# Performance work log

Hardware: AMD Instinct MI355X
Metric: run time of the kernel (lower is better)

The kernel has to match this reference:

```python
import jax, jax.numpy as jnp
import numpy as np

EMB = 2048
NH = 16
HD = EMB // NH
EPS = 1e-5


def setup_inputs() -> dict:
    key = jax.random.key(0)
    ks = jax.random.split(key, 16)
    s = 1.0 / np.sqrt(EMB)
    def lin(k, din, dout):
        return jax.random.normal(k, (din, dout), jnp.float32) * (1.0 / np.sqrt(din))
    return {
        "embeddings": jax.random.normal(ks[0], (2, 2048, EMB), jnp.float32),
        "Wq": lin(ks[1], EMB, EMB), "bq": jnp.zeros((EMB,), jnp.float32),
        "Wk": lin(ks[2], EMB, EMB), "bk": jnp.zeros((EMB,), jnp.float32),
        "Wv": lin(ks[3], EMB, EMB), "bv": jnp.zeros((EMB,), jnp.float32),
        "Wfc": lin(ks[4], EMB, EMB), "bfc": jnp.zeros((EMB,), jnp.float32),
        "g1": jnp.ones((EMB,), jnp.float32), "be1": jnp.zeros((EMB,), jnp.float32),
        "W1": lin(ks[5], EMB, 4 * EMB), "b1": jnp.zeros((4 * EMB,), jnp.float32),
        "W2": lin(ks[6], 4 * EMB, EMB), "b2": jnp.zeros((EMB,), jnp.float32),
        "g2": jnp.ones((EMB,), jnp.float32), "be2": jnp.zeros((EMB,), jnp.float32),
    }


def _layernorm(x, g, b):
    mu = jnp.mean(x, axis=-1, keepdims=True)
    var = jnp.mean(jnp.square(x - mu), axis=-1, keepdims=True)
    return (x - mu) * jax.lax.rsqrt(var + EPS) * g + b


def reference(embeddings, Wq, bq, Wk, bk, Wv, bv, Wfc, bfc, g1, be1, W1, b1, W2, b2, g2, be2):
    B, S, E = embeddings.shape
    old = embeddings
    # QKV projections, split heads: [B, H, S, D]
    def heads(x):
        return x.reshape(B, S, NH, HD).transpose(0, 2, 1, 3)
    q = heads(embeddings @ Wq + bq)
    k = heads(embeddings @ Wk + bk)
    v = heads(embeddings @ Wv + bv)
    # naive causal attention: full [B,H,S,S] scores (faithful to source)
    scores = jnp.einsum("bhsd,bhtd->bhst", q, k) / np.sqrt(HD)
    causal = jnp.triu(jnp.full((S, S), -jnp.inf, jnp.float32), k=1)
    scores = scores + causal[None, None]
    attn = jax.nn.softmax(scores, axis=-1)
    ctx = jnp.einsum("bhst,bhtd->bhsd", attn, v)
    ctx = ctx.transpose(0, 2, 1, 3).reshape(B, S, E)
    # dropout is identity in eval mode
    x = ctx @ Wfc + bfc + old
    old = _layernorm(x, g1, be1)
    h = jax.nn.gelu(old @ W1 + b1, approximate=False)
    x = h @ W2 + b2 + old
    return _layernorm(x, g2, be2)
```

## Files before the change

kernel.cpp:

```cpp
#include <hip/hip_runtime.h>
#include <hip/hip_bf16.h>
#include <math.h>

#define EMB  2048
#define NH   16
#define HD   128
#define SEQ  2048
#define BATCH 2
#define MTOK (BATCH*SEQ)

using bf16x8 = __attribute__((ext_vector_type(8))) __bf16;
using f32x4  = __attribute__((ext_vector_type(4))) float;

__device__ __forceinline__ unsigned short f2bf(float x) {
    unsigned int u = __float_as_uint(x);
    u += 0x7fffu + ((u >> 16) & 1u);
    return (unsigned short)(u >> 16);
}

__device__ __forceinline__ float gelu_exact(float x) {
    return 0.5f * x * (1.0f + erff(x * 0.70710678118654752f));
}

__global__ __launch_bounds__(256) void k_conv(const float* __restrict__ in,
                                              unsigned short* __restrict__ out, int n4) {
    int i = blockIdx.x * 256 + threadIdx.x;
    if (i >= n4) return;
    float4 v = ((const float4*)in)[i];
    ushort4 o;
    o.x = f2bf(v.x); o.y = f2bf(v.y); o.z = f2bf(v.z); o.w = f2bf(v.w);
    ((ushort4*)out)[i] = o;
}

__global__ __launch_bounds__(256) void k_transconv(const float* __restrict__ W,
                                                   unsigned short* __restrict__ Wt,
                                                   int K, int N) {
    __shared__ float t[32][33];
    int tx = threadIdx.x & 31, ty = threadIdx.x >> 5;
    int c0 = blockIdx.x * 32, r0 = blockIdx.y * 32;
    #pragma unroll
    for (int i = 0; i < 4; ++i)
        t[ty + i*8][tx] = W[(size_t)(r0 + ty + i*8) * N + c0 + tx];
    __syncthreads();
    #pragma unroll
    for (int i = 0; i < 4; ++i)
        Wt[(size_t)(c0 + ty + i*8) * K + r0 + tx] = f2bf(t[tx][ty + i*8]);
}

template<int EPI, int NSPLIT>
__global__ __launch_bounds__(512, 1) void k_gemm3(const unsigned short* __restrict__ A,
                                                  const unsigned short* __restrict__ Bt,
                                                  const float* __restrict__ bias,
                                                  void* __restrict__ C0,
                                                  void* __restrict__ C1,
                                                  void* __restrict__ C2,
                                                  int M, int N, int Kred, int ldk) {
    __shared__ unsigned short As[2][256 * 64];
    __shared__ unsigned short Bs[2][256 * 64];
    const int tid = threadIdx.x, lane = tid & 63, wid = tid >> 6;
    const int wm = wid >> 2, wn = wid & 3;
    const int nmt = M >> 8, nnt = N >> 8;
    const int nblk = nmt * nnt * NSPLIT, cpx = nblk >> 3;
    const int swz = (blockIdx.x & 7) * cpx + (blockIdx.x >> 3);
    const int bm = swz % nmt;
    const int t2 = swz / nmt;
    const int bn = t2 % nnt, kk = t2 / nnt;
    const unsigned short* Ab = A  + (size_t)bm * 256 * ldk + (size_t)kk * Kred;
    const unsigned short* Bb = Bt + (size_t)bn * 256 * ldk + (size_t)kk * Kred;

    auto STAGE = [&](int ti, int bbuf) {
        const int kt = ti * 64;
        #pragma unroll
        for (int it = 0; it < 4; ++it) {
            const int slot = it * 512 + tid;
            const int r = slot >> 3, cs = slot & 7;
            const unsigned short* ga = Ab + (size_t)r * ldk + kt + ((cs ^ (r & 7)) * 8);
            __builtin_amdgcn_global_load_lds(
                (const __attribute__((address_space(1))) void*)ga,
                (__attribute__((address_space(3))) void*)&As[bbuf][(it*512 + wid*64) * 8], 16, 0, 0);
            const unsigned short* gb = Bb + (size_t)r * ldk + kt + ((cs ^ (r & 7)) * 8);
            __builtin_amdgcn_global_load_lds(
                (const __attribute__((address_space(1))) void*)gb,
                (__attribute__((address_space(3))) void*)&Bs[bbuf][(it*512 + wid*64) * 8], 16, 0, 0);
        }
    };

    f32x4 acc[8][4] = {};
    const int NT = Kred >> 6;
    STAGE(0, 0);
    STAGE(1, 1);

    for (int t = 0; t < NT; ++t) {
        const int bb = t & 1;
        if (t == NT - 1) asm volatile("s_waitcnt vmcnt(0)" ::: "memory");
        else             asm volatile("s_waitcnt vmcnt(8)" ::: "memory");
        __builtin_amdgcn_s_barrier();
        __builtin_amdgcn_sched_barrier(0);

        #pragma unroll
        for (int kh = 0; kh < 2; ++kh) {
            bf16x8 af[8], bfr[4];
            #pragma unroll
            for (int mi = 0; mi < 8; ++mi)
                af[mi] = *(const bf16x8*)&As[bb][(wm*128 + mi*16 + (lane & 15))*64
                                                + (((kh*4 + (lane >> 4)) ^ (lane & 7)) * 8)];
            #pragma unroll
            for (int ni = 0; ni < 4; ++ni)
                bfr[ni] = *(const bf16x8*)&Bs[bb][(wn*64 + ni*16 + (lane & 15))*64
                                                 + (((kh*4 + (lane >> 4)) ^ (lane & 7)) * 8)];
            __builtin_amdgcn_s_setprio(1);
            #pragma unroll
            for (int mi = 0; mi < 8; ++mi)
                #pragma unroll
                for (int ni = 0; ni < 4; ++ni)
                    acc[mi][ni] = __builtin_amdgcn_mfma_f32_16x16x32_bf16(af[mi], bfr[ni], acc[mi][ni], 0, 0, 0);
            __builtin_amdgcn_s_setprio(0);
            __builtin_amdgcn_sched_barrier(0);
        }

        __builtin_amdgcn_s_barrier();
        __builtin_amdgcn_sched_barrier(0);
        if (t + 2 < NT) STAGE(t + 2, bb);
    }

    const int row0b = bm*256 + wm*128, col0 = bn*256 + wn*64;
    #pragma unroll
    for (int mi = 0; mi < 8; ++mi) {
        #pragma unroll
        for (int ni = 0; ni < 4; ++ni) {
            const int c = col0 + ni*16 + (lane & 15);
            const int r0 = row0b + mi*16 + (lane >> 4) * 4;
            if (EPI == 5) {
                float* out = (float*)C0 + (size_t)kk * M * N;
                #pragma unroll
                for (int j = 0; j < 4; ++j)
                    out[(size_t)(r0+j) * N + c] = acc[mi][ni][j];
            } else if (EPI == 2) {
                const float bv = bias[c];
                #pragma unroll
                for (int j = 0; j < 4; ++j)
                    ((unsigned short*)C0)[(size_t)(r0+j) * N + c] = f2bf(gelu_exact(acc[mi][ni][j] + bv));
            } else {
                const float bv = bias[c];
                const int seg = c >> 11;
                if (seg == 0) {
                    #pragma unroll
                    for (int j = 0; j < 4; ++j)
                        ((unsigned short*)C0)[(size_t)(r0+j) * EMB + c] = f2bf(acc[mi][ni][j] + bv);
                } else if (seg == 1) {
                    #pragma unroll
                    for (int j = 0; j < 4; ++j)
                        ((unsigned short*)C1)[(size_t)(r0+j) * EMB + (c - 2048)] = f2bf(acc[mi][ni][j] + bv);
                } else {
                    const int cc = c - 4096;
                    const int hh = cc >> 7, dd = cc & 127;
                    const int bb2 = r0 >> 11, s0 = r0 & 2047;
                    ushort4 u;
                    u.x = f2bf(acc[mi][ni][0] + bv); u.y = f2bf(acc[mi][ni][1] + bv);
                    u.z = f2bf(acc[mi][ni][2] + bv); u.w = f2bf(acc[mi][ni][3] + bv);
                    *(ushort4*)((unsigned short*)C2 +
                                ((size_t)((bb2*NH + hh)*HD + dd) * SEQ + s0)) = u;
                }
            }
        }
    }
}

__global__ __launch_bounds__(256, 4) void k_attn_part(const unsigned short* __restrict__ Qb,
                                                      const unsigned short* __restrict__ Kb,
                                                      const unsigned short* __restrict__ VTb,
                                                      float* __restrict__ Opart,
                                                      float* __restrict__ Ml) {
    const int tid = threadIdx.x;
    const int lane = tid & 63, w = tid >> 6;
    const int g = lane >> 4, c = lane & 15;
    const int bid = blockIdx.x;
    const int swz = (bid & 7) * 512 + (bid >> 3);
    const int bh = swz >> 7;
    const int b = bh >> 4, h = bh & 15;
    const int rr = swz & 127;
    const int qt = rr >> 2, ks = rr & 3;
    const int nt = qt + 1;
    const int t0 = (nt * ks) >> 2, t1 = (nt * (ks + 1)) >> 2;
    const int qb = qt * 64 + w * 16;

    __shared__ unsigned short Ks[64 * 128];
    __shared__ unsigned short Vs[128 * 64];
    __shared__ unsigned short p_lds[4][16 * 64];

    bf16x8 qf[4];
    {
        const unsigned short* qrow = Qb + (size_t)(b*SEQ + qb + c) * EMB + h*HD;
        #pragma unroll
        for (int dch = 0; dch < 4; ++dch)
            qf[dch] = *(const bf16x8*)(qrow + dch*32 + g*8);
    }

    f32x4 o[8];
    #pragma unroll
    for (int ni = 0; ni < 8; ++ni) o[ni] = (f32x4){0.f, 0.f, 0.f, 0.f};
    float m_c = -1e30f, l_c = 0.f;

    const int q = qb + c;
    const int qmaxw = qb + 15;
    const unsigned short* Kbase = Kb  + (size_t)(b*SEQ) * EMB + h*HD;
    const unsigned short* Vbase = VTb + (size_t)((b*NH + h) * HD) * SEQ;
    const float scale = 0.08838834764831845f;
    char* pw = (char*)&p_lds[w][0];

    for (int ti = t0; ti < t1; ++ti) {
        const int tc = ti * 64;
        #pragma unroll
        for (int it = 0; it < 4; ++it) {
            const int cl = it * 256 + tid;
            const unsigned short* gk = Kbase + (size_t)(tc + (cl >> 4)) * EMB
                                     + (((cl & 15) ^ ((cl >> 4) & 7)) * 8);
            __builtin_amdgcn_global_load_lds(
                (const __attribute__((address_space(1))) void*)gk,
                (__attribute__((address_space(3))) void*)&Ks[(it*256 + w*64) * 8], 16, 0, 0);
            const unsigned short* gv = Vbase + (size_t)(cl >> 3) * SEQ + tc
                                     + (((cl & 7) ^ ((cl >> 3) & 7)) * 8);
            __builtin_amdgcn_global_load_lds(
                (const __attribute__((address_space(1))) void*)gv,
                (__attribute__((address_space(3))) void*)&Vs[(it*256 + w*64) * 8], 16, 0, 0);
        }
        __syncthreads();

        f32x4 sc[4];
        #pragma unroll
        for (int kt = 0; kt < 4; ++kt) {
            sc[kt] = (f32x4){0.f, 0.f, 0.f, 0.f};
            if (tc + kt*16 <= qmaxw) {
                #pragma unroll
                for (int dch = 0; dch < 4; ++dch) {
                    bf16x8 kf = *(const bf16x8*)&Ks[(kt*16 + c)*128 + (((dch*4 + g) ^ (c & 7)) * 8)];
                    sc[kt] = __builtin_amdgcn_mfma_f32_16x16x32_bf16(kf, qf[dch], sc[kt], 0, 0, 0);
                }
            }
        }
        float mx = -1e30f;
        #pragma unroll
        for (int kt = 0; kt < 4; ++kt)
            #pragma unroll
            for (int j = 0; j < 4; ++j) {
                const int key = tc + kt*16 + g*4 + j;
                const float s = (key <= q) ? sc[kt][j] * scale : -1e30f;
                mx = fmaxf(mx, s);
            }
        mx = fmaxf(mx, __shfl_xor(mx, 16));
        mx = fmaxf(mx, __shfl_xor(mx, 32));
        if (!__all(mx <= m_c + 8.f)) {
            const float mn = fmaxf(m_c, mx);
            const float corr = __expf(m_c - mn);
            l_c *= corr;
            m_c = mn;
            #pragma unroll
            for (int j = 0; j < 4; ++j) {
                const float cj = __shfl(corr, g*4 + j);
                #pragma unroll
                for (int ni = 0; ni < 8; ++ni) o[ni][j] *= cj;
            }
        }
        float ps = 0.f;
        #pragma unroll
        for (int kt = 0; kt < 4; ++kt) {
            float p[4];
            #pragma unroll
            for (int j = 0; j < 4; ++j) {
                const int key = tc + kt*16 + g*4 + j;
                const float s = (key <= q) ? sc[kt][j] * scale : -1e30f;
                p[j] = __expf(s - m_c);
                ps += p[j];
            }
            uint2 pk;
            pk.x = (unsigned int)f2bf(p[0]) | ((unsigned int)f2bf(p[1]) << 16);
            pk.y = (unsigned int)f2bf(p[2]) | ((unsigned int)f2bf(p[3]) << 16);
            const int byte = (c*128 + kt*32 + g*8) ^ ((c & 7) << 4);
            *(uint2*)(pw + byte) = pk;
        }
        ps += __shfl_xor(ps, 16);
        ps += __shfl_xor(ps, 32);
        l_c += ps;
        asm volatile("s_waitcnt lgkmcnt(0)" ::: "memory");
        __builtin_amdgcn_sched_barrier(0);
        #pragma unroll
        for (int kc = 0; kc < 2; ++kc) {
            if (tc + kc*32 <= qmaxw) {
                const int byte = (c*128 + kc*64 + g*16) ^ ((c & 7) << 4);
                bf16x8 pa = *(const bf16x8*)(pw + byte);
                #pragma unroll
                for (int ni = 0; ni < 8; ++ni) {
                    bf16x8 vf = *(const bf16x8*)&Vs[(ni*16 + c)*64 + (((kc*4 + g) ^ (c & 7)) * 8)];
                    o[ni] = __builtin_amdgcn_mfma_f32_16x16x32_bf16(pa, vf, o[ni], 0, 0, 0);
                }
            }
        }
        __syncthreads();
    }

    const int slot = ((b*NH + h) * 32 + qt) * 4 + ks;
    float* op = Opart + (size_t)slot * (64 * 128);
    #pragma unroll
    for (int ni = 0; ni < 8; ++ni)
        #pragma unroll
        for (int j = 0; j < 4; ++j)
            op[(size_t)(w*16 + g*4 + j) * 128 + ni*16 + c] = o[ni][j];
    if (lane < 16) {
        Ml[(size_t)slot * 128 +      w*16 + lane] = m_c;
        Ml[(size_t)slot * 128 + 64 + w*16 + lane] = l_c;
    }
}

__global__ __launch_bounds__(256) void k_attn_reduce(const float* __restrict__ Opart,
                                                     const float* __restrict__ Ml,
                                                     unsigned short* __restrict__ Ob) {
    const int qt = blockIdx.x, h = blockIdx.y, b = blockIdx.z;
    const int slot0 = ((b*NH + h) * 32 + qt) * 4;
    const int row = threadIdx.x >> 2;
    const int c0 = (threadIdx.x & 3) * 32;
    float M = -1e30f;
    #pragma unroll
    for (int s = 0; s < 4; ++s)
        M = fmaxf(M, Ml[(size_t)(slot0 + s) * 128 + row]);
    float L = 0.f;
    float wgt[4];
    #pragma unroll
    for (int s = 0; s < 4; ++s) {
        wgt[s] = __expf(Ml[(size_t)(slot0 + s) * 128 + row] - M);
        L += Ml[(size_t)(slot0 + s) * 128 + 64 + row] * wgt[s];
    }
    float acc[32];
    #pragma unroll
    for (int k = 0; k < 32; ++k) acc[k] = 0.f;
    #pragma unroll
    for (int s = 0; s < 4; ++s) {
        const float4* op = (const float4*)(Opart + ((size_t)(slot0 + s) * 64 + row) * 128 + c0);
        #pragma unroll
        for (int q4 = 0; q4 < 8; ++q4) {
            float4 v = op[q4];
            acc[q4*4+0] += v.x * wgt[s]; acc[q4*4+1] += v.y * wgt[s];
            acc[q4*4+2] += v.z * wgt[s]; acc[q4*4+3] += v.w * wgt[s];
        }
    }
    const float inv = 1.0f / L;
    unsigned short* orow = Ob + (size_t)(b*SEQ + qt*64 + row) * EMB + h*HD + c0;
    #pragma unroll
    for (int q4 = 0; q4 < 8; ++q4) {
        ushort4 u;
        u.x = f2bf(acc[q4*4+0] * inv); u.y = f2bf(acc[q4*4+1] * inv);
        u.z = f2bf(acc[q4*4+2] * inv); u.w = f2bf(acc[q4*4+3] * inv);
        ((ushort4*)orow)[q4] = u;
    }
}

__global__ __launch_bounds__(256) void k_ln(const float* __restrict__ X0,
                                            const float* __restrict__ X1,
                                            const float* __restrict__ bias,
                                            const float* __restrict__ res,
                                            const float* __restrict__ g,
                                            const float* __restrict__ be,
                                            float* __restrict__ Of32,
                                            unsigned short* __restrict__ Obf16) {
    const int row = blockIdx.x;
    float4 v[2];
    float s = 0.f, ss = 0.f;
    #pragma unroll
    for (int i = 0; i < 2; ++i) {
        const int c4 = threadIdx.x + i*256;
        float4 a = ((const float4*)(X0 + (size_t)row * EMB))[c4];
        if (X1) {
            float4 b1v = ((const float4*)(X1 + (size_t)row * EMB))[c4];
            a.x += b1v.x; a.y += b1v.y; a.z += b1v.z; a.w += b1v.w;
        }
        if (bias) {
            float4 bv = ((const float4*)bias)[c4];
            a.x += bv.x; a.y += bv.y; a.z += bv.z; a.w += bv.w;
        }
        if (res) {
            float4 rv = ((const float4*)(res + (size_t)row * EMB))[c4];
            a.x += rv.x; a.y += rv.y; a.z += rv.z; a.w += rv.w;
        }
        v[i] = a;
        s  += a.x + a.y + a.z + a.w;
        ss += a.x*a.x + a.y*a.y + a.z*a.z + a.w*a.w;
    }
    #pragma unroll
    for (int o = 32; o; o >>= 1) { s += __shfl_xor(s, o); ss += __shfl_xor(ss, o); }
    __shared__ float red[2][4];
    const int lane = threadIdx.x & 63, wid = threadIdx.x >> 6;
    if (lane == 0) { red[0][wid] = s; red[1][wid] = ss; }
    __syncthreads();
    s  = red[0][0] + red[0][1] + red[0][2] + red[0][3];
    ss = red[1][0] + red[1][1] + red[1][2] + red[1][3];
    const float mu = s * (1.0f / EMB);
    const float var = ss * (1.0f / EMB) - mu * mu;
    const float rs = rsqrtf(var + 1e-5f);
    #pragma unroll
    for (int i = 0; i < 2; ++i) {
        const int c4 = threadIdx.x + i*256;
        float4 gv = ((const float4*)g)[c4];
        float4 bv = ((const float4*)be)[c4];
        float4 y;
        y.x = (v[i].x - mu) * rs * gv.x + bv.x;
        y.y = (v[i].y - mu) * rs * gv.y + bv.y;
        y.z = (v[i].z - mu) * rs * gv.z + bv.z;
        y.w = (v[i].w - mu) * rs * gv.w + bv.w;
        if (Of32)  ((float4*)(Of32 + (size_t)row * EMB))[c4] = y;
        if (Obf16) {
            ushort4 u; u.x = f2bf(y.x); u.y = f2bf(y.y); u.z = f2bf(y.z); u.w = f2bf(y.w);
            ((ushort4*)(Obf16 + (size_t)row * EMB))[c4] = u;
        }
    }
}

extern "C" void kernel_launch(void* const* d_in, const int* in_sizes, int n_in,
                              void* d_out, int out_size, void* d_ws, size_t ws_size,
                              hipStream_t stream) {
    const float* emb = (const float*)d_in[0];
    const float* Wq  = (const float*)d_in[1];  const float* bq  = (const float*)d_in[2];
    const float* Wk  = (const float*)d_in[3];  const float* bk  = (const float*)d_in[4];
    const float* Wv  = (const float*)d_in[5];  const float* bv  = (const float*)d_in[6];
    const float* Wfc = (const float*)d_in[7];  const float* bfc = (const float*)d_in[8];
    const float* g1  = (const float*)d_in[9];  const float* be1 = (const float*)d_in[10];
    const float* W1  = (const float*)d_in[11]; const float* b1  = (const float*)d_in[12];
    const float* W2  = (const float*)d_in[13]; const float* b2  = (const float*)d_in[14];
    const float* g2  = (const float*)d_in[15]; const float* be2 = (const float*)d_in[16];

    char* ws = (char*)d_ws;
    unsigned short* aB   = (unsigned short*)(ws + (size_t)  0 * (1u<<20));
    unsigned short* ln1B = (unsigned short*)(ws + (size_t) 16 * (1u<<20));
    unsigned short* WtB  = (unsigned short*)(ws + (size_t) 32 * (1u<<20));
    float*          Ml   = (float*)         (ws + (size_t) 32 * (1u<<20));
    unsigned short* hB   = (unsigned short*)(ws + (size_t) 64 * (1u<<20));
    unsigned short* Qb   = (unsigned short*)(ws + (size_t) 64 * (1u<<20));
    unsigned short* Kb   = (unsigned short*)(ws + (size_t) 80 * (1u<<20));
    unsigned short* VTb  = (unsigned short*)(ws + (size_t) 96 * (1u<<20));
    float*          Opart= (float*)         (ws + (size_t)112 * (1u<<20));
    float*          pA   = (float*)         (ws + (size_t)128 * (1u<<20));
    float*          ln1f = (float*)         (ws + (size_t)192 * (1u<<20));
    float*          bias6= (float*)         (ws + (size_t)236 * (1u<<20));

    const dim3 blk(256);
    const dim3 blk2(512);
    const int n4 = MTOK * EMB / 4;

    k_conv<<<dim3(n4 / 256), blk, 0, stream>>>(emb, aB, n4);
    hipMemcpyAsync(bias6,        bq, EMB*sizeof(float), hipMemcpyDeviceToDevice, stream);
    hipMemcpyAsync(bias6 + EMB,  bk, EMB*sizeof(float), hipMemcpyDeviceToDevice, stream);
    hipMemcpyAsync(bias6 + 2*EMB,bv, EMB*sizeof(float), hipMemcpyDeviceToDevice, stream);

    k_transconv<<<dim3(EMB/32, EMB/32), blk, 0, stream>>>(Wq, WtB,              EMB, EMB);
    k_transconv<<<dim3(EMB/32, EMB/32), blk, 0, stream>>>(Wk, WtB + EMB*EMB,    EMB, EMB);
    k_transconv<<<dim3(EMB/32, EMB/32), blk, 0, stream>>>(Wv, WtB + 2*EMB*EMB,  EMB, EMB);
    k_gemm3<6,1><<<dim3((MTOK/256)*(3*EMB/256)), blk2, 0, stream>>>(
        aB, WtB, bias6, Qb, Kb, VTb, MTOK, 3*EMB, EMB, EMB);

    k_attn_part<<<dim3(4096), blk, 0, stream>>>(Qb, Kb, VTb, Opart, Ml);
    k_attn_reduce<<<dim3(SEQ/64, NH, BATCH), blk, 0, stream>>>(Opart, Ml, aB);

    k_transconv<<<dim3(EMB/32, EMB/32), blk, 0, stream>>>(Wfc, WtB, EMB, EMB);
    k_gemm3<5,2><<<dim3((MTOK/256)*(EMB/256)*2), blk2, 0, stream>>>(
        aB, WtB, nullptr, pA, nullptr, nullptr, MTOK, EMB, EMB/2, EMB);
    k_ln<<<dim3(MTOK), blk, 0, stream>>>(pA, pA + (size_t)MTOK*EMB, bfc, emb, g1, be1, ln1f, ln1B);

    k_transconv<<<dim3(4*EMB/32, EMB/32), blk, 0, stream>>>(W1, WtB, EMB, 4*EMB);
    k_gemm3<2,1><<<dim3((MTOK/256)*(4*EMB/256)), blk2, 0, stream>>>(
        ln1B, WtB, b1, hB, nullptr, nullptr, MTOK, 4*EMB, EMB, EMB);

    k_transconv<<<dim3(EMB/32, (4*EMB)/32), blk, 0, stream>>>(W2, WtB, 4*EMB, EMB);
    k_gemm3<5,2><<<dim3((MTOK/256)*(EMB/256)*2), blk2, 0, stream>>>(
        hB, WtB, nullptr, pA, nullptr, nullptr, MTOK, EMB, 2*EMB, 4*EMB);
    k_ln<<<dim3(MTOK), blk, 0, stream>>>(pA, pA + (size_t)MTOK*EMB, b2, ln1f, g2, be2, (float*)d_out, nullptr);
}
```

Baseline: 818.4 us.

## Split GEMM K-tile into half-stages with interleaved load/MFMA ping-pong schedule

```diff
diff --git a/kernel.cpp b/kernel.cpp
--- a/kernel.cpp
+++ b/kernel.cpp
@@ -55,8 +55,8 @@
                                                   void* __restrict__ C1,
                                                   void* __restrict__ C2,
                                                   int M, int N, int Kred, int ldk) {
-    __shared__ unsigned short As[2][256 * 64];
-    __shared__ unsigned short Bs[2][256 * 64];
+    __shared__ unsigned short As[2][2][256 * 32];
+    __shared__ unsigned short Bs[2][2][256 * 32];
     const int tid = threadIdx.x, lane = tid & 63, wid = tid >> 6;
     const int wm = wid >> 2, wn = wid & 3;
     const int nmt = M >> 8, nnt = N >> 8;
@@ -64,63 +64,117 @@
     const int swz = (blockIdx.x & 7) * cpx + (blockIdx.x >> 3);
     const int bm = swz % nmt;
     const int t2 = swz / nmt;
-    const int bn = t2 % nnt, kk = t2 / nnt;
-    const unsigned short* Ab = A  + (size_t)bm * 256 * ldk + (size_t)kk * Kred;
-    const unsigned short* Bb = Bt + (size_t)bn * 256 * ldk + (size_t)kk * Kred;
-
-    auto STAGE = [&](int ti, int bbuf) {
-        const int kt = ti * 64;
-        #pragma unroll
-        for (int it = 0; it < 4; ++it) {
-            const int slot = it * 512 + tid;
-            const int r = slot >> 3, cs = slot & 7;
-            const unsigned short* ga = Ab + (size_t)r * ldk + kt + ((cs ^ (r & 7)) * 8);
-            __builtin_amdgcn_global_load_lds(
-                (const __attribute__((address_space(1))) void*)ga,
-                (__attribute__((address_space(3))) void*)&As[bbuf][(it*512 + wid*64) * 8], 16, 0, 0);
-            const unsigned short* gb = Bb + (size_t)r * ldk + kt + ((cs ^ (r & 7)) * 8);
-            __builtin_amdgcn_global_load_lds(
-                (const __attribute__((address_space(1))) void*)gb,
-                (__attribute__((address_space(3))) void*)&Bs[bbuf][(it*512 + wid*64) * 8], 16, 0, 0);
-        }
+    const int bn = t2 % nnt, kk2 = t2 / nnt;
+    const unsigned short* Ab = A  + (size_t)bm * 256 * ldk + (size_t)kk2 * Kred;
+    const unsigned short* Bb = Bt + (size_t)bn * 256 * ldk + (size_t)kk2 * Kred;
+
+    const int sr0 = tid >> 2,        sc0 = (tid & 3) ^ ((sr0 >> 1) & 3);
+    const int sr1 = (512 + tid) >> 2, sc1 = ((512 + tid) & 3) ^ ((sr1 >> 1) & 3);
+
+    auto STAGE = [&](const unsigned short* gb, int u, int kh, unsigned short* lds) {
+        const int kb = u * 64 + kh * 32;
+        __builtin_amdgcn_global_load_lds(
+            (const __attribute__((address_space(1))) void*)(gb + (size_t)sr0 * ldk + kb + sc0 * 8),
+            (__attribute__((address_space(3))) void*)&lds[(size_t)wid * 64 * 8], 16, 0, 0);
+        __builtin_amdgcn_global_load_lds(
+            (const __attribute__((address_space(1))) void*)(gb + (size_t)sr1 * ldk + kb + sc1 * 8),
+            (__attribute__((address_space(3))) void*)&lds[(size_t)(512 + wid * 64) * 8], 16, 0, 0);
     };
+
+    const int ck   = (((lane >> 4) ^ ((lane >> 1) & 3)) * 8);
+    const int la15 = lane & 15;
 
     f32x4 acc[8][4] = {};
     const int NT = Kred >> 6;
-    STAGE(0, 0);
-    STAGE(1, 1);
-
-    for (int t = 0; t < NT; ++t) {
-        const int bb = t & 1;
-        if (t == NT - 1) asm volatile("s_waitcnt vmcnt(0)" ::: "memory");
-        else             asm volatile("s_waitcnt vmcnt(8)" ::: "memory");
-        __builtin_amdgcn_s_barrier();
-        __builtin_amdgcn_sched_barrier(0);
-
-        #pragma unroll
-        for (int kh = 0; kh < 2; ++kh) {
-            bf16x8 af[8], bfr[4];
-            #pragma unroll
-            for (int mi = 0; mi < 8; ++mi)
-                af[mi] = *(const bf16x8*)&As[bb][(wm*128 + mi*16 + (lane & 15))*64
-                                                + (((kh*4 + (lane >> 4)) ^ (lane & 7)) * 8)];
-            #pragma unroll
-            for (int ni = 0; ni < 4; ++ni)
-                bfr[ni] = *(const bf16x8*)&Bs[bb][(wn*64 + ni*16 + (lane & 15))*64
-                                                 + (((kh*4 + (lane >> 4)) ^ (lane & 7)) * 8)];
-            __builtin_amdgcn_s_setprio(1);
-            #pragma unroll
-            for (int mi = 0; mi < 8; ++mi)
-                #pragma unroll
-                for (int ni = 0; ni < 4; ++ni)
-                    acc[mi][ni] = __builtin_amdgcn_mfma_f32_16x16x32_bf16(af[mi], bfr[ni], acc[mi][ni], 0, 0, 0);
-            __builtin_amdgcn_s_setprio(0);
-            __builtin_amdgcn_sched_barrier(0);
-        }
-
-        __builtin_amdgcn_s_barrier();
-        __builtin_amdgcn_sched_barrier(0);
-        if (t + 2 < NT) STAGE(t + 2, bb);
+
+    STAGE(Ab, 0, 0, &As[0][0][0]);
+    STAGE(Bb, 0, 0, &Bs[0][0][0]);
+    STAGE(Ab, 0, 1, &As[0][1][0]);
+    STAGE(Bb, 0, 1, &Bs[0][1][0]);
+    asm volatile("s_waitcnt vmcnt(4)" ::: "memory");
+    __builtin_amdgcn_s_barrier();
+
+    for (int u = 0; u < NT; ++u) {
+        const int cur = u & 1, nb = cur ^ 1;
+        const bool more = (u + 1 < NT);
+        bf16x8 af[8], bfr[4];
+
+        #pragma unroll
+        for (int mi = 0; mi < 8; ++mi)
+            af[mi] = *(const bf16x8*)&As[cur][0][(wm*128 + mi*16 + la15)*32 + ck];
+        bfr[0] = *(const bf16x8*)&Bs[cur][0][(wn*64 +  0 + la15)*32 + ck];
+        bfr[1] = *(const bf16x8*)&Bs[cur][0][(wn*64 + 16 + la15)*32 + ck];
+        if (more) STAGE(Ab, u + 1, 0, &As[nb][0][0]);
+        __builtin_amdgcn_sched_barrier(0);
+        __builtin_amdgcn_s_barrier();
+        asm volatile("s_waitcnt lgkmcnt(0)" ::: "memory");
+        __builtin_amdgcn_sched_barrier(0);
+        __builtin_amdgcn_s_setprio(1);
+        #pragma unroll
+        for (int mi = 0; mi < 8; ++mi) {
+            acc[mi][0] = __builtin_amdgcn_mfma_f32_16x16x32_bf16(af[mi], bfr[0], acc[mi][0], 0, 0, 0);
+            acc[mi][1] = __builtin_amdgcn_mfma_f32_16x16x32_bf16(af[mi], bfr[1], acc[mi][1], 0, 0, 0);
+        }
+        __builtin_amdgcn_s_setprio(0);
+        __builtin_amdgcn_sched_barrier(0);
+        __builtin_amdgcn_s_barrier();
+
+        bfr[2] = *(const bf16x8*)&Bs[cur][0][(wn*64 + 32 + la15)*32 + ck];
+        bfr[3] = *(const bf16x8*)&Bs[cur][0][(wn*64 + 48 + la15)*32 + ck];
+        if (more) STAGE(Bb, u + 1, 0, &Bs[nb][0][0]);
+        __builtin_amdgcn_sched_barrier(0);
+        __builtin_amdgcn_s_barrier();
+        asm volatile("s_waitcnt lgkmcnt(0)" ::: "memory");
+        __builtin_amdgcn_sched_barrier(0);
+        __builtin_amdgcn_s_setprio(1);
+        #pragma unroll
+        for (int mi = 0; mi < 8; ++mi) {
+            acc[mi][2] = __builtin_amdgcn_mfma_f32_16x16x32_bf16(af[mi], bfr[2], acc[mi][2], 0, 0, 0);
+            acc[mi][3] = __builtin_amdgcn_mfma_f32_16x16x32_bf16(af[mi], bfr[3], acc[mi][3], 0, 0, 0);
+        }
+        __builtin_amdgcn_s_setprio(0);
+        __builtin_amdgcn_sched_barrier(0);
+        if (more) asm volatile("s_waitcnt vmcnt(4)" ::: "memory");
+        else      asm volatile("s_waitcnt vmcnt(0)" ::: "memory");
+        __builtin_amdgcn_s_barrier();
+
+        #pragma unroll
+        for (int mi = 0; mi < 8; ++mi)
+            af[mi] = *(const bf16x8*)&As[cur][1][(wm*128 + mi*16 + la15)*32 + ck];
+        bfr[0] = *(const bf16x8*)&Bs[cur][1][(wn*64 +  0 + la15)*32 + ck];
+        bfr[1] = *(const bf16x8*)&Bs[cur][1][(wn*64 + 16 + la15)*32 + ck];
+        if (more) STAGE(Ab, u + 1, 1, &As[nb][1][0]);
+        __builtin_amdgcn_sched_barrier(0);
+        __builtin_amdgcn_s_barrier();
+        asm volatile("s_waitcnt lgkmcnt(0)" ::: "memory");
+        __builtin_amdgcn_sched_barrier(0);
+        __builtin_amdgcn_s_setprio(1);
+        #pragma unroll
+        for (int mi = 0; mi < 8; ++mi) {
+            acc[mi][0] = __builtin_amdgcn_mfma_f32_16x16x32_bf16(af[mi], bfr[0], acc[mi][0], 0, 0, 0);
+            acc[mi][1] = __builtin_amdgcn_mfma_f32_16x16x32_bf16(af[mi], bfr[1], acc[mi][1], 0, 0, 0);
+        }
+        __builtin_amdgcn_s_setprio(0);
+        __builtin_amdgcn_sched_barrier(0);
+        __builtin_amdgcn_s_barrier();
+
+        bfr[2] = *(const bf16x8*)&Bs[cur][1][(wn*64 + 32 + la15)*32 + ck];
+        bfr[3] = *(const bf16x8*)&Bs[cur][1][(wn*64 + 48 + la15)*32 + ck];
+        if (more) STAGE(Bb, u + 1, 1, &Bs[nb][1][0]);
+        __builtin_amdgcn_sched_barrier(0);
+        __builtin_amdgcn_s_barrier();
+        asm volatile("s_waitcnt lgkmcnt(0)" ::: "memory");
+        __builtin_amdgcn_sched_barrier(0);
+        __builtin_amdgcn_s_setprio(1);
+        #pragma unroll
+        for (int mi = 0; mi < 8; ++mi) {
+            acc[mi][2] = __builtin_amdgcn_mfma_f32_16x16x32_bf16(af[mi], bfr[2], acc[mi][2], 0, 0, 0);
+            acc[mi][3] = __builtin_amdgcn_mfma_f32_16x16x32_bf16(af[mi], bfr[3], acc[mi][3], 0, 0, 0);
+        }
+        __builtin_amdgcn_s_setprio(0);
+        __builtin_amdgcn_sched_barrier(0);
+        asm volatile("s_waitcnt vmcnt(4)" ::: "memory");
+        __builtin_amdgcn_s_barrier();
     }
 
     const int row0b = bm*256 + wm*128, col0 = bn*256 + wn*64;
@@ -128,10 +182,10 @@
     for (int mi = 0; mi < 8; ++mi) {
         #pragma unroll
         for (int ni = 0; ni < 4; ++ni) {
-            const int c = col0 + ni*16 + (lane & 15);
+            const int c = col0 + ni*16 + la15;
             const int r0 = row0b + mi*16 + (lane >> 4) * 4;
             if (EPI == 5) {
-                float* out = (float*)C0 + (size_t)kk * M * N;
+                float* out = (float*)C0 + (size_t)kk2 * M * N;
                 #pragma unroll
                 for (int j = 0; j < 4; ++j)
                     out[(size_t)(r0+j) * N + c] = acc[mi][ni][j];
@@ -155,11 +209,11 @@
                     const int cc = c - 4096;
                     const int hh = cc >> 7, dd = cc & 127;
                     const int bb2 = r0 >> 11, s0 = r0 & 2047;
-                    ushort4 u;
-                    u.x = f2bf(acc[mi][ni][0] + bv); u.y = f2bf(acc[mi][ni][1] + bv);
-                    u.z = f2bf(acc[mi][ni][2] + bv); u.w = f2bf(acc[mi][ni][3] + bv);
+                    ushort4 uo;
+                    uo.x = f2bf(acc[mi][ni][0] + bv); uo.y = f2bf(acc[mi][ni][1] + bv);
+                    uo.z = f2bf(acc[mi][ni][2] + bv); uo.w = f2bf(acc[mi][ni][3] + bv);
                     *(ushort4*)((unsigned short*)C2 +
-                                ((size_t)((bb2*NH + hh)*HD + dd) * SEQ + s0)) = u;
+                                ((size_t)((bb2*NH + hh)*HD + dd) * SEQ + s0)) = uo;
                 }
             }
         }
```

Result: no change. 830.5 us (+1.5%).

## Pre-pack weights into MFMA fragment layout and load B directly to registers

Applied to the files above, without the earlier changes.

```diff
diff --git a/kernel.cpp b/kernel.cpp
--- a/kernel.cpp
+++ b/kernel.cpp
@@ -32,9 +32,9 @@
     ((ushort4*)out)[i] = o;
 }
 
-__global__ __launch_bounds__(256) void k_transconv(const float* __restrict__ W,
-                                                   unsigned short* __restrict__ Wt,
-                                                   int K, int N) {
+__global__ __launch_bounds__(256) void k_transpack(const float* __restrict__ W,
+                                                   unsigned short* __restrict__ Bp,
+                                                   int K, int N, int noff) {
     __shared__ float t[32][33];
     int tx = threadIdx.x & 31, ty = threadIdx.x >> 5;
     int c0 = blockIdx.x * 32, r0 = blockIdx.y * 32;
@@ -42,85 +42,110 @@
     for (int i = 0; i < 4; ++i)
         t[ty + i*8][tx] = W[(size_t)(r0 + ty + i*8) * N + c0 + tx];
     __syncthreads();
-    #pragma unroll
-    for (int i = 0; i < 4; ++i)
-        Wt[(size_t)(c0 + ty + i*8) * K + r0 + tx] = f2bf(t[tx][ty + i*8]);
+    const int kc = r0 >> 5;
+    #pragma unroll
+    for (int i = 0; i < 4; ++i) {
+        const int ng = noff + c0 + ty + i*8;
+        Bp[((size_t)(ng >> 4) * (K >> 5) + kc) * 512 + (ng & 15) * 32 + tx] =
+            f2bf(t[tx][ty + i*8]);
+    }
 }
 
 template<int EPI, int NSPLIT>
-__global__ __launch_bounds__(512, 1) void k_gemm3(const unsigned short* __restrict__ A,
-                                                  const unsigned short* __restrict__ Bt,
+__global__ __launch_bounds__(512, 1) void k_gemm4(const unsigned short* __restrict__ A,
+                                                  const unsigned short* __restrict__ Bp,
                                                   const float* __restrict__ bias,
                                                   void* __restrict__ C0,
                                                   void* __restrict__ C1,
                                                   void* __restrict__ C2,
                                                   int M, int N, int Kred, int ldk) {
     __shared__ unsigned short As[2][256 * 64];
-    __shared__ unsigned short Bs[2][256 * 64];
     const int tid = threadIdx.x, lane = tid & 63, wid = tid >> 6;
+    const int la15 = lane & 15, g = lane >> 4;
     const int wm = wid >> 2, wn = wid & 3;
     const int nmt = M >> 8, nnt = N >> 8;
     const int nblk = nmt * nnt * NSPLIT, cpx = nblk >> 3;
     const int swz = (blockIdx.x & 7) * cpx + (blockIdx.x >> 3);
     const int bm = swz % nmt;
     const int t2 = swz / nmt;
-    const int bn = t2 % nnt, kk = t2 / nnt;
-    const unsigned short* Ab = A  + (size_t)bm * 256 * ldk + (size_t)kk * Kred;
-    const unsigned short* Bb = Bt + (size_t)bn * 256 * ldk + (size_t)kk * Kred;
-
-    auto STAGE = [&](int ti, int bbuf) {
-        const int kt = ti * 64;
+    const int bn = t2 % nnt, kk2 = t2 / nnt;
+    const unsigned short* Ab = A + (size_t)bm * 256 * ldk + (size_t)kk2 * Kred;
+    const int nkc = ldk >> 5;
+    const unsigned short* Bptr = Bp + ((size_t)(bn*16 + wn*4) * nkc + ((kk2 * Kred) >> 5)) * 512
+                               + la15 * 32 + g * 8;
+
+    auto STAGE_A = [&](int tt, int bbuf) {
+        const int kt = tt * 64;
         #pragma unroll
         for (int it = 0; it < 4; ++it) {
-            const int slot = it * 512 + tid;
-            const int r = slot >> 3, cs = slot & 7;
-            const unsigned short* ga = Ab + (size_t)r * ldk + kt + ((cs ^ (r & 7)) * 8);
+            const int r = it * 64 + (tid >> 3);
+            const int cs = (tid & 7) ^ (r & 7);
             __builtin_amdgcn_global_load_lds(
-                (const __attribute__((address_space(1))) void*)ga,
+                (const __attribute__((address_space(1))) void*)(Ab + (size_t)r * ldk + kt + cs * 8),
                 (__attribute__((address_space(3))) void*)&As[bbuf][(it*512 + wid*64) * 8], 16, 0, 0);
-            const unsigned short* gb = Bb + (size_t)r * ldk + kt + ((cs ^ (r & 7)) * 8);
-            __builtin_amdgcn_global_load_lds(
-                (const __attribute__((address_space(1))) void*)gb,
-                (__attribute__((address_space(3))) void*)&Bs[bbuf][(it*512 + wid*64) * 8], 16, 0, 0);
-        }
+        }
+    };
+
+    bf16x8 bregA[4], bregB[4];
+    auto BLOADA = [&](int tt, int kh) {
+        #pragma unroll
+        for (int ni = 0; ni < 4; ++ni)
+            bregA[ni] = *(const bf16x8*)(Bptr + ((size_t)ni * nkc + tt*2 + kh) * 512);
+    };
+    auto BLOADB = [&](int tt, int kh) {
+        #pragma unroll
+        for (int ni = 0; ni < 4; ++ni)
+            bregB[ni] = *(const bf16x8*)(Bptr + ((size_t)ni * nkc + tt*2 + kh) * 512);
     };
 
     f32x4 acc[8][4] = {};
     const int NT = Kred >> 6;
-    STAGE(0, 0);
-    STAGE(1, 1);
+
+    STAGE_A(0, 0);
+    __builtin_amdgcn_sched_barrier(0);
+    BLOADA(0, 0);
+    __builtin_amdgcn_sched_barrier(0);
+    STAGE_A(1, 1);
+    asm volatile("s_waitcnt vmcnt(8)" ::: "memory");
+    __builtin_amdgcn_s_barrier();
 
     for (int t = 0; t < NT; ++t) {
-        const int bb = t & 1;
-        if (t == NT - 1) asm volatile("s_waitcnt vmcnt(0)" ::: "memory");
-        else             asm volatile("s_waitcnt vmcnt(8)" ::: "memory");
-        __builtin_amdgcn_s_barrier();
-        __builtin_amdgcn_sched_barrier(0);
-
-        #pragma unroll
-        for (int kh = 0; kh < 2; ++kh) {
-            bf16x8 af[8], bfr[4];
-            #pragma unroll
-            for (int mi = 0; mi < 8; ++mi)
-                af[mi] = *(const bf16x8*)&As[bb][(wm*128 + mi*16 + (lane & 15))*64
-                                                + (((kh*4 + (lane >> 4)) ^ (lane & 7)) * 8)];
+        const int cur = t & 1;
+        if (t + 1 < NT) asm volatile("s_waitcnt vmcnt(4)" ::: "memory");
+        else            asm volatile("s_waitcnt vmcnt(0)" ::: "memory");
+
+        BLOADB(t, 1);
+
+        bf16x8 af[8];
+        #pragma unroll
+        for (int mi = 0; mi < 8; ++mi)
+            af[mi] = *(const bf16x8*)&As[cur][(wm*128 + mi*16 + la15)*64 + ((g ^ (lane & 7)) * 8)];
+        __builtin_amdgcn_s_setprio(1);
+        #pragma unroll
+        for (int mi = 0; mi < 8; ++mi)
             #pragma unroll
             for (int ni = 0; ni < 4; ++ni)
-                bfr[ni] = *(const bf16x8*)&Bs[bb][(wn*64 + ni*16 + (lane & 15))*64
-                                                 + (((kh*4 + (lane >> 4)) ^ (lane & 7)) * 8)];
-            __builtin_amdgcn_s_setprio(1);
+                acc[mi][ni] = __builtin_amdgcn_mfma_f32_16x16x32_bf16(af[mi], bregA[ni], acc[mi][ni], 0, 0, 0);
+        __builtin_amdgcn_s_setprio(0);
+
+        asm volatile("s_waitcnt vmcnt(0)" ::: "memory");
+
+        #pragma unroll
+        for (int mi = 0; mi < 8; ++mi)
+            af[mi] = *(const bf16x8*)&As[cur][(wm*128 + mi*16 + la15)*64 + (((4 + g) ^ (lane & 7)) * 8)];
+        __builtin_amdgcn_s_setprio(1);
+        #pragma unroll
+        for (int mi = 0; mi < 8; ++mi)
             #pragma unroll
-            for (int mi = 0; mi < 8; ++mi)
-                #pragma unroll
-                for (int ni = 0; ni < 4; ++ni)
-                    acc[mi][ni] = __builtin_amdgcn_mfma_f32_16x16x32_bf16(af[mi], bfr[ni], acc[mi][ni], 0, 0, 0);
-            __builtin_amdgcn_s_setprio(0);
-            __builtin_amdgcn_sched_barrier(0);
-        }
-
+            for (int ni = 0; ni < 4; ++ni)
+                acc[mi][ni] = __builtin_amdgcn_mfma_f32_16x16x32_bf16(af[mi], bregB[ni], acc[mi][ni], 0, 0, 0);
+        __builtin_amdgcn_s_setprio(0);
+
+        __builtin_amdgcn_sched_barrier(0);
         __builtin_amdgcn_s_barrier();
+        if (t + 1 < NT) BLOADA(t + 1, 0);
         __builtin_amdgcn_sched_barrier(0);
-        if (t + 2 < NT) STAGE(t + 2, bb);
+        if (t + 2 < NT) STAGE_A(t + 2, cur);
     }
 
     const int row0b = bm*256 + wm*128, col0 = bn*256 + wn*64;
@@ -128,10 +153,10 @@
     for (int mi = 0; mi < 8; ++mi) {
         #pragma unroll
         for (int ni = 0; ni < 4; ++ni) {
-            const int c = col0 + ni*16 + (lane & 15);
-            const int r0 = row0b + mi*16 + (lane >> 4) * 4;
+            const int c = col0 + ni*16 + la15;
+            const int r0 = row0b + mi*16 + g * 4;
             if (EPI == 5) {
-                float* out = (float*)C0 + (size_t)kk * M * N;
+                float* out = (float*)C0 + (size_t)kk2 * M * N;
                 #pragma unroll
                 for (int j = 0; j < 4; ++j)
                     out[(size_t)(r0+j) * N + c] = acc[mi][ni][j];
@@ -155,11 +180,11 @@
                     const int cc = c - 4096;
                     const int hh = cc >> 7, dd = cc & 127;
                     const int bb2 = r0 >> 11, s0 = r0 & 2047;
-                    ushort4 u;
-                    u.x = f2bf(acc[mi][ni][0] + bv); u.y = f2bf(acc[mi][ni][1] + bv);
-                    u.z = f2bf(acc[mi][ni][2] + bv); u.w = f2bf(acc[mi][ni][3] + bv);
+                    ushort4 uo;
+                    uo.x = f2bf(acc[mi][ni][0] + bv); uo.y = f2bf(acc[mi][ni][1] + bv);
+                    uo.z = f2bf(acc[mi][ni][2] + bv); uo.w = f2bf(acc[mi][ni][3] + bv);
                     *(ushort4*)((unsigned short*)C2 +
-                                ((size_t)((bb2*NH + hh)*HD + dd) * SEQ + s0)) = u;
+                                ((size_t)((bb2*NH + hh)*HD + dd) * SEQ + s0)) = uo;
                 }
             }
         }
@@ -449,26 +474,26 @@
     hipMemcpyAsync(bias6 + EMB,  bk, EMB*sizeof(float), hipMemcpyDeviceToDevice, stream);
     hipMemcpyAsync(bias6 + 2*EMB,bv, EMB*sizeof(float), hipMemcpyDeviceToDevice, stream);
 
-    k_transconv<<<dim3(EMB/32, EMB/32), blk, 0, stream>>>(Wq, WtB,              EMB, EMB);
-    k_transconv<<<dim3(EMB/32, EMB/32), blk, 0, stream>>>(Wk, WtB + EMB*EMB,    EMB, EMB);
-    k_transconv<<<dim3(EMB/32, EMB/32), blk, 0, stream>>>(Wv, WtB + 2*EMB*EMB,  EMB, EMB);
-    k_gemm3<6,1><<<dim3((MTOK/256)*(3*EMB/256)), blk2, 0, stream>>>(
+    k_transpack<<<dim3(EMB/32, EMB/32), blk, 0, stream>>>(Wq, WtB, EMB, EMB, 0);
+    k_transpack<<<dim3(EMB/32, EMB/32), blk, 0, stream>>>(Wk, WtB, EMB, EMB, 2048);
+    k_transpack<<<dim3(EMB/32, EMB/32), blk, 0, stream>>>(Wv, WtB, EMB, EMB, 4096);
+    k_gemm4<6,1><<<dim3((MTOK/256)*(3*EMB/256)), blk2, 0, stream>>>(
         aB, WtB, bias6, Qb, Kb, VTb, MTOK, 3*EMB, EMB, EMB);
 
     k_attn_part<<<dim3(4096), blk, 0, stream>>>(Qb, Kb, VTb, Opart, Ml);
     k_attn_reduce<<<dim3(SEQ/64, NH, BATCH), blk, 0, stream>>>(Opart, Ml, aB);
 
-    k_transconv<<<dim3(EMB/32, EMB/32), blk, 0, stream>>>(Wfc, WtB, EMB, EMB);
-    k_gemm3<5,2><<<dim3((MTOK/256)*(EMB/256)*2), blk2, 0, stream>>>(
+    k_transpack<<<dim3(EMB/32, EMB/32), blk, 0, stream>>>(Wfc, WtB, EMB, EMB, 0);
+    k_gemm4<5,2><<<dim3((MTOK/256)*(EMB/256)*2), blk2, 0, stream>>>(
         aB, WtB, nullptr, pA, nullptr, nullptr, MTOK, EMB, EMB/2, EMB);
     k_ln<<<dim3(MTOK), blk, 0, stream>>>(pA, pA + (size_t)MTOK*EMB, bfc, emb, g1, be1, ln1f, ln1B);
 
-    k_transconv<<<dim3(4*EMB/32, EMB/32), blk, 0, stream>>>(W1, WtB, EMB, 4*EMB);
-    k_gemm3<2,1><<<dim3((MTOK/256)*(4*EMB/256)), blk2, 0, stream>>>(
+    k_transpack<<<dim3(4*EMB/32, EMB/32), blk, 0, stream>>>(W1, WtB, EMB, 4*EMB, 0);
+    k_gemm4<2,1><<<dim3((MTOK/256)*(4*EMB/256)), blk2, 0, stream>>>(
         ln1B, WtB, b1, hB, nullptr, nullptr, MTOK, 4*EMB, EMB, EMB);
 
-    k_transconv<<<dim3(EMB/32, (4*EMB)/32), blk, 0, stream>>>(W2, WtB, 4*EMB, EMB);
-    k_gemm3<5,2><<<dim3((MTOK/256)*(EMB/256)*2), blk2, 0, stream>>>(
+    k_transpack<<<dim3(EMB/32, (4*EMB)/32), blk, 0, stream>>>(W2, WtB, 4*EMB, EMB, 0);
+    k_gemm4<5,2><<<dim3((MTOK/256)*(EMB/256)*2), blk2, 0, stream>>>(
         hB, WtB, nullptr, pA, nullptr, nullptr, MTOK, EMB, 2*EMB, 4*EMB);
     k_ln<<<dim3(MTOK), blk, 0, stream>>>(pA, pA + (size_t)MTOK*EMB, b2, ln1f, g2, be2, (float*)d_out, nullptr);
 }
```

Result: slower. 874.0 us (+6.8%).

## Store split-K partials, attention partials and LN1 residual in bf16

Applied to the files above, without the earlier changes.

```diff
diff --git a/kernel.cpp b/kernel.cpp
--- a/kernel.cpp
+++ b/kernel.cpp
@@ -16,6 +16,9 @@
     unsigned int u = __float_as_uint(x);
     u += 0x7fffu + ((u >> 16) & 1u);
     return (unsigned short)(u >> 16);
+}
+__device__ __forceinline__ float bf2f(unsigned int u16) {
+    return __uint_as_float(u16 << 16);
 }
 
 __device__ __forceinline__ float gelu_exact(float x) {
@@ -64,9 +67,9 @@
     const int swz = (blockIdx.x & 7) * cpx + (blockIdx.x >> 3);
     const int bm = swz % nmt;
     const int t2 = swz / nmt;
-    const int bn = t2 % nnt, kk = t2 / nnt;
-    const unsigned short* Ab = A  + (size_t)bm * 256 * ldk + (size_t)kk * Kred;
-    const unsigned short* Bb = Bt + (size_t)bn * 256 * ldk + (size_t)kk * Kred;
+    const int bn = t2 % nnt, kk2 = t2 / nnt;
+    const unsigned short* Ab = A  + (size_t)bm * 256 * ldk + (size_t)kk2 * Kred;
+    const unsigned short* Bb = Bt + (size_t)bn * 256 * ldk + (size_t)kk2 * Kred;
 
     auto STAGE = [&](int ti, int bbuf) {
         const int kt = ti * 64;
@@ -131,10 +134,10 @@
             const int c = col0 + ni*16 + (lane & 15);
             const int r0 = row0b + mi*16 + (lane >> 4) * 4;
             if (EPI == 5) {
-                float* out = (float*)C0 + (size_t)kk * M * N;
+                unsigned short* out = (unsigned short*)C0 + (size_t)kk2 * M * N;
                 #pragma unroll
                 for (int j = 0; j < 4; ++j)
-                    out[(size_t)(r0+j) * N + c] = acc[mi][ni][j];
+                    out[(size_t)(r0+j) * N + c] = f2bf(acc[mi][ni][j]);
             } else if (EPI == 2) {
                 const float bv = bias[c];
                 #pragma unroll
@@ -155,11 +158,11 @@
                     const int cc = c - 4096;
                     const int hh = cc >> 7, dd = cc & 127;
                     const int bb2 = r0 >> 11, s0 = r0 & 2047;
-                    ushort4 u;
-                    u.x = f2bf(acc[mi][ni][0] + bv); u.y = f2bf(acc[mi][ni][1] + bv);
-                    u.z = f2bf(acc[mi][ni][2] + bv); u.w = f2bf(acc[mi][ni][3] + bv);
+                    ushort4 uo;
+                    uo.x = f2bf(acc[mi][ni][0] + bv); uo.y = f2bf(acc[mi][ni][1] + bv);
+                    uo.z = f2bf(acc[mi][ni][2] + bv); uo.w = f2bf(acc[mi][ni][3] + bv);
                     *(ushort4*)((unsigned short*)C2 +
-                                ((size_t)((bb2*NH + hh)*HD + dd) * SEQ + s0)) = u;
+                                ((size_t)((bb2*NH + hh)*HD + dd) * SEQ + s0)) = uo;
                 }
             }
         }
@@ -169,7 +172,7 @@
 __global__ __launch_bounds__(256, 4) void k_attn_part(const unsigned short* __restrict__ Qb,
                                                       const unsigned short* __restrict__ Kb,
                                                       const unsigned short* __restrict__ VTb,
-                                                      float* __restrict__ Opart,
+                                                      unsigned short* __restrict__ Opart,
                                                       float* __restrict__ Ml) {
     const int tid = threadIdx.x;
     const int lane = tid & 63, w = tid >> 6;
@@ -299,19 +302,19 @@
     }
 
     const int slot = ((b*NH + h) * 32 + qt) * 4 + ks;
-    float* op = Opart + (size_t)slot * (64 * 128);
+    unsigned short* op = Opart + (size_t)slot * (64 * 128);
     #pragma unroll
     for (int ni = 0; ni < 8; ++ni)
         #pragma unroll
         for (int j = 0; j < 4; ++j)
-            op[(size_t)(w*16 + g*4 + j) * 128 + ni*16 + c] = o[ni][j];
+            op[(size_t)(w*16 + g*4 + j) * 128 + ni*16 + c] = f2bf(o[ni][j]);
     if (lane < 16) {
         Ml[(size_t)slot * 128 +      w*16 + lane] = m_c;
         Ml[(size_t)slot * 128 + 64 + w*16 + lane] = l_c;
     }
 }
 
-__global__ __launch_bounds__(256) void k_attn_reduce(const float* __restrict__ Opart,
+__global__ __launch_bounds__(256) void k_attn_reduce(const unsigned short* __restrict__ Opart,
                                                      const float* __restrict__ Ml,
                                                      unsigned short* __restrict__ Ob) {
     const int qt = blockIdx.x, h = blockIdx.y, b = blockIdx.z;
@@ -334,12 +337,16 @@
     for (int k = 0; k < 32; ++k) acc[k] = 0.f;
     #pragma unroll
     for (int s = 0; s < 4; ++s) {
-        const float4* op = (const float4*)(Opart + ((size_t)(slot0 + s) * 64 + row) * 128 + c0);
-        #pragma unroll
-        for (int q4 = 0; q4 < 8; ++q4) {
-            float4 v = op[q4];
-            acc[q4*4+0] += v.x * wgt[s]; acc[q4*4+1] += v.y * wgt[s];
-            acc[q4*4+2] += v.z * wgt[s]; acc[q4*4+3] += v.w * wgt[s];
+        const unsigned short* op = Opart + ((size_t)(slot0 + s) * 64 + row) * 128 + c0;
+        #pragma unroll
+        for (int q4 = 0; q4 < 4; ++q4) {
+            uint4 u = ((const uint4*)op)[q4];
+            const unsigned int* pu = (const unsigned int*)&u;
+            #pragma unroll
+            for (int k = 0; k < 4; ++k) {
+                acc[q4*8 + 2*k]     += bf2f(pu[k] & 0xffffu) * wgt[s];
+                acc[q4*8 + 2*k + 1] += bf2f(pu[k] >> 16)     * wgt[s];
+            }
         }
     }
     const float inv = 1.0f / L;
@@ -353,41 +360,55 @@
     }
 }
 
-__global__ __launch_bounds__(256) void k_ln(const float* __restrict__ X0,
-                                            const float* __restrict__ X1,
-                                            const float* __restrict__ bias,
-                                            const float* __restrict__ res,
-                                            const float* __restrict__ g,
-                                            const float* __restrict__ be,
-                                            float* __restrict__ Of32,
-                                            unsigned short* __restrict__ Obf16) {
-    const int row = blockIdx.x;
-    float4 v[2];
+__global__ __launch_bounds__(256) void k_lnb(const unsigned short* __restrict__ X0,
+                                             const unsigned short* __restrict__ X1,
+                                             const float* __restrict__ bias,
+                                             const float* __restrict__ resF,
+                                             const unsigned short* __restrict__ resB,
+                                             const float* __restrict__ g,
+                                             const float* __restrict__ be,
+                                             float* __restrict__ Of32,
+                                             unsigned short* __restrict__ Obf16) {
+    const int row = blockIdx.x, t = threadIdx.x;
+    float v[8];
+    {
+        uint4 a = ((const uint4*)(X0 + (size_t)row * EMB))[t];
+        uint4 b = ((const uint4*)(X1 + (size_t)row * EMB))[t];
+        const unsigned int* pa = (const unsigned int*)&a;
+        const unsigned int* pb = (const unsigned int*)&b;
+        #pragma unroll
+        for (int i = 0; i < 4; ++i) {
+            v[2*i]   = bf2f(pa[i] & 0xffffu) + bf2f(pb[i] & 0xffffu);
+            v[2*i+1] = bf2f(pa[i] >> 16)     + bf2f(pb[i] >> 16);
+        }
+    }
+    {
+        float4 b0 = ((const float4*)bias)[t*2], b1 = ((const float4*)bias)[t*2+1];
+        v[0] += b0.x; v[1] += b0.y; v[2] += b0.z; v[3] += b0.w;
+        v[4] += b1.x; v[5] += b1.y; v[6] += b1.z; v[7] += b1.w;
+    }
+    if (resF) {
+        float4 r0 = ((const float4*)(resF + (size_t)row * EMB))[t*2];
+        float4 r1 = ((const float4*)(resF + (size_t)row * EMB))[t*2+1];
+        v[0] += r0.x; v[1] += r0.y; v[2] += r0.z; v[3] += r0.w;
+        v[4] += r1.x; v[5] += r1.y; v[6] += r1.z; v[7] += r1.w;
+    }
+    if (resB) {
+        uint4 r = ((const uint4*)(resB + (size_t)row * EMB))[t];
+        const unsigned int* pr = (const unsigned int*)&r;
+        #pragma unroll
+        for (int i = 0; i < 4; ++i) {
+            v[2*i]   += bf2f(pr[i] & 0xffffu);
+            v[2*i+1] += bf2f(pr[i] >> 16);
+        }
+    }
     float s = 0.f, ss = 0.f;
     #pragma unroll
-    for (int i = 0; i < 2; ++i) {
-        const int c4 = threadIdx.x + i*256;
-        float4 a = ((const float4*)(X0 + (size_t)row * EMB))[c4];
-        if (X1) {
-            float4 b1v = ((const float4*)(X1 + (size_t)row * EMB))[c4];
-            a.x += b1v.x; a.y += b1v.y; a.z += b1v.z; a.w += b1v.w;
-        }
-        if (bias) {
-            float4 bv = ((const float4*)bias)[c4];
-            a.x += bv.x; a.y += bv.y; a.z += bv.z; a.w += bv.w;
-        }
-        if (res) {
-            float4 rv = ((const float4*)(res + (size_t)row * EMB))[c4];
-            a.x += rv.x; a.y += rv.y; a.z += rv.z; a.w += rv.w;
-        }
-        v[i] = a;
-        s  += a.x + a.y + a.z + a.w;
-        ss += a.x*a.x + a.y*a.y + a.z*a.z + a.w*a.w;
-    }
+    for (int i = 0; i < 8; ++i) { s += v[i]; ss += v[i]*v[i]; }
     #pragma unroll
     for (int o = 32; o; o >>= 1) { s += __shfl_xor(s, o); ss += __shfl_xor(ss, o); }
     __shared__ float red[2][4];
-    const int lane = threadIdx.x & 63, wid = threadIdx.x >> 6;
+    const int lane = t & 63, wid = t >> 6;
     if (lane == 0) { red[0][wid] = s; red[1][wid] = ss; }
     __syncthreads();
     s  = red[0][0] + red[0][1] + red[0][2] + red[0][3];
@@ -395,21 +416,32 @@
     const float mu = s * (1.0f / EMB);
     const float var = ss * (1.0f / EMB) - mu * mu;
     const float rs = rsqrtf(var + 1e-5f);
-    #pragma unroll
-    for (int i = 0; i < 2; ++i) {
-        const int c4 = threadIdx.x + i*256;
-        float4 gv = ((const float4*)g)[c4];
-        float4 bv = ((const float4*)be)[c4];
-        float4 y;
-        y.x = (v[i].x - mu) * rs * gv.x + bv.x;
-        y.y = (v[i].y - mu) * rs * gv.y + bv.y;
-        y.z = (v[i].z - mu) * rs * gv.z + bv.z;
-        y.w = (v[i].w - mu) * rs * gv.w + bv.w;
-        if (Of32)  ((float4*)(Of32 + (size_t)row * EMB))[c4] = y;
-        if (Obf16) {
-            ushort4 u; u.x = f2bf(y.x); u.y = f2bf(y.y); u.z = f2bf(y.z); u.w = f2bf(y.w);
-            ((ushort4*)(Obf16 + (size_t)row * EMB))[c4] = u;
-        }
+    float y[8];
+    {
+        float4 g0 = ((const float4*)g)[t*2],  g1v = ((const float4*)g)[t*2+1];
+        float4 e0 = ((const float4*)be)[t*2], e1 = ((const float4*)be)[t*2+1];
+        const float* pg0 = (const float*)&g0; const float* pg1 = (const float*)&g1v;
+        const float* pe0 = (const float*)&e0; const float* pe1 = (const float*)&e1;
+        #pragma unroll
+        for (int i = 0; i < 4; ++i) {
+            y[i]   = (v[i]   - mu) * rs * pg0[i] + pe0[i];
+            y[i+4] = (v[i+4] - mu) * rs * pg1[i] + pe1[i];
+        }
+    }
+    if (Of32) {
+        float4 o0, o1;
+        o0.x = y[0]; o0.y = y[1]; o0.z = y[2]; o0.w = y[3];
+        o1.x = y[4]; o1.y = y[5]; o1.z = y[6]; o1.w = y[7];
+        ((float4*)(Of32 + (size_t)row * EMB))[t*2]   = o0;
+        ((float4*)(Of32 + (size_t)row * EMB))[t*2+1] = o1;
+    }
+    if (Obf16) {
+        uint4 u;
+        unsigned int* pu = (unsigned int*)&u;
+        #pragma unroll
+        for (int i = 0; i < 4; ++i)
+            pu[i] = (unsigned int)f2bf(y[2*i]) | ((unsigned int)f2bf(y[2*i+1]) << 16);
+        ((uint4*)(Obf16 + (size_t)row * EMB))[t] = u;
     }
 }
 
@@ -435,9 +467,8 @@
     unsigned short* Qb   = (unsigned short*)(ws + (size_t) 64 * (1u<<20));
     unsigned short* Kb   = (unsigned short*)(ws + (size_t) 80 * (1u<<20));
     unsigned short* VTb  = (unsigned short*)(ws + (size_t) 96 * (1u<<20));
-    float*          Opart= (float*)         (ws + (size_t)112 * (1u<<20));
-    float*          pA   = (float*)         (ws + (size_t)128 * (1u<<20));
-    float*          ln1f = (float*)         (ws + (size_t)192 * (1u<<20));
+    unsigned short* Opart= (unsigned short*)(ws + (size_t)112 * (1u<<20));
+    unsigned short* pA   = (unsigned short*)(ws + (size_t)176 * (1u<<20));
     float*          bias6= (float*)         (ws + (size_t)236 * (1u<<20));
 
     const dim3 blk(256);
@@ -461,7 +492,8 @@
     k_transconv<<<dim3(EMB/32, EMB/32), blk, 0, stream>>>(Wfc, WtB, EMB, EMB);
     k_gemm3<5,2><<<dim3((MTOK/256)*(EMB/256)*2), blk2, 0, stream>>>(
         aB, WtB, nullptr, pA, nullptr, nullptr, MTOK, EMB, EMB/2, EMB);
-    k_ln<<<dim3(MTOK), blk, 0, stream>>>(pA, pA + (size_t)MTOK*EMB, bfc, emb, g1, be1, ln1f, ln1B);
+    k_lnb<<<dim3(MTOK), blk, 0, stream>>>(pA, pA + (size_t)MTOK*EMB, bfc, emb, nullptr,
+                                          g1, be1, nullptr, ln1B);
 
     k_transconv<<<dim3(4*EMB/32, EMB/32), blk, 0, stream>>>(W1, WtB, EMB, 4*EMB);
     k_gemm3<2,1><<<dim3((MTOK/256)*(4*EMB/256)), blk2, 0, stream>>>(
@@ -470,5 +502,6 @@
     k_transconv<<<dim3(EMB/32, (4*EMB)/32), blk, 0, stream>>>(W2, WtB, 4*EMB, EMB);
     k_gemm3<5,2><<<dim3((MTOK/256)*(EMB/256)*2), blk2, 0, stream>>>(
         hB, WtB, nullptr, pA, nullptr, nullptr, MTOK, EMB, 2*EMB, 4*EMB);
-    k_ln<<<dim3(MTOK), blk, 0, stream>>>(pA, pA + (size_t)MTOK*EMB, b2, ln1f, g2, be2, (float*)d_out, nullptr);
-}
+    k_lnb<<<dim3(MTOK), blk, 0, stream>>>(pA, pA + (size_t)MTOK*EMB, b2, nullptr, ln1B,
+                                          g2, be2, (float*)d_out, nullptr);
+}
```

New measurement: 681.2 us. 1.2x faster.
